# Performance work log

Hardware: AMD Instinct MI355X
Metric: run time of the kernel (lower is better)

The kernel has to match this reference:

```python
import jax, jax.numpy as jnp
import numpy as np
from jax import lax

B, H, V, L = 128, 256, 130, 100  # batch, hidden_size, vocab per stream, decode length


def _gru(x, h, wih, whh, bih, bhh):
    # torch.nn.GRUCell math
    gi = x @ wih.T + bih
    gh = h @ whh.T + bhh
    ir, iz, inn = jnp.split(gi, 3, axis=-1)
    hr, hz, hn = jnp.split(gh, 3, axis=-1)
    r = jax.nn.sigmoid(ir + hr)
    u = jax.nn.sigmoid(iz + hz)
    n = jnp.tanh(inn + r * hn)
    return (1.0 - u) * n + u * h


def _forward(z, gru1_wih, gru1_whh, gru1_bih, gru1_bhh,
             gru2_wih, gru2_whh, gru2_bih, gru2_bhh,
             ctx_wih, ctx_whh, ctx_bih, ctx_bhh,
             out_w, out_b, hid_w, hid_b, emb, length):
    b = z.shape[0]
    hidden = jnp.tanh(z @ hid_w.T + hid_b)                      # [B,H]
    h3 = jnp.broadcast_to(hidden[None], (3, b, hidden.shape[-1]))
    note0 = jnp.broadcast_to(emb[:, 0][:, None, :], (3, b, emb.shape[-1]))  # embed index 0
    vgru = jax.vmap(_gru)  # over the 3 parallel streams

    def step(carry, _):
        g1h, g2h, context, note = carry
        zb = jnp.broadcast_to(z[None], note.shape)
        g1h = vgru(jnp.concatenate([note, zb], -1), g1h,
                   gru1_wih, gru1_whh, gru1_bih, gru1_bhh)       # [3,B,H]
        unroll = g1h
        logits = []
        for i in range(3):  # fixed structural unroll (3 streams)
            ctx_in = jnp.concatenate([unroll[0], unroll[1], unroll[2]], -1)  # [B,3H]
            context = _gru(ctx_in, context, ctx_wih, ctx_whh, ctx_bih, ctx_bhh)
            h2 = _gru(jnp.concatenate([context, z], -1), g2h[i],
                      gru2_wih[i], gru2_whh[i], gru2_bih[i], gru2_bhh[i])
            g2h = g2h.at[i].set(h2)
            lg = (unroll[i] + h2) @ out_w[i].T + out_b[i]        # [B,V]
            logits.append(lg)
            ni = emb[i][jnp.argmax(lg, axis=-1)]                 # greedy sample -> embed
            note = note.at[i].set(ni)
            # NOTE: original code uses self.gru1[1] here (fixed index 1) -- kept faithful
            unroll = unroll.at[i].set(_gru(jnp.concatenate([ni, z], -1), unroll[i],
                                           gru1_wih[1], gru1_whh[1], gru1_bih[1], gru1_bhh[1]))
        return (g1h, g2h, context, note), jnp.stack(logits)     # [3,B,V]

    _, ys = lax.scan(step, (h3, h3, hidden, note0), None, length=length)
    return jnp.transpose(ys, (1, 2, 0, 3))                      # [3,B,L,V]


def setup_inputs() -> dict:
    key = jax.random.key(0)
    ks = jax.random.split(key, 18)
    s = 0.05
    n = lambda k, shp: jax.random.normal(k, shp, jnp.float32) * s
    return {
        "z": jax.random.normal(ks[0], (B, H), jnp.float32),
        "gru1_wih": n(ks[1], (3, 3 * H, 2 * H)),
        "gru1_whh": n(ks[2], (3, 3 * H, H)),
        "gru1_bih": n(ks[3], (3, 3 * H)),
        "gru1_bhh": n(ks[4], (3, 3 * H)),
        "gru2_wih": n(ks[5], (3, 3 * H, 2 * H)),
        "gru2_whh": n(ks[6], (3, 3 * H, H)),
        "gru2_bih": n(ks[7], (3, 3 * H)),
        "gru2_bhh": n(ks[8], (3, 3 * H)),
        "ctx_wih": n(ks[9], (3 * H, 3 * H)),
        "ctx_whh": n(ks[10], (3 * H, H)),
        "ctx_bih": n(ks[11], (3 * H,)),
        "ctx_bhh": n(ks[12], (3 * H,)),
        "out_w": n(ks[13], (3, V, H)),
        "out_b": n(ks[14], (3, V)),
        "hid_w": n(ks[15], (H, H)),
        "hid_b": n(ks[16], (H,)),
        "emb": n(ks[17], (3, V, H)),
        "length": L,
    }


def reference(z, gru1_wih, gru1_whh, gru1_bih, gru1_bhh,
              gru2_wih, gru2_whh, gru2_bih, gru2_bhh,
              ctx_wih, ctx_whh, ctx_bih, ctx_bhh,
              out_w, out_b, hid_w, hid_b, emb, length):
    return _forward(z, gru1_wih, gru1_whh, gru1_bih, gru1_bhh,
                    gru2_wih, gru2_whh, gru2_bih, gru2_bhh,
                    ctx_wih, ctx_whh, ctx_bih, ctx_bhh,
                    out_w, out_b, hid_w, hid_b, emb, length)
```

## Files before the change

### kernel.cpp

```cpp
#include <hip/hip_runtime.h>
#include <math.h>

#define B 128
#define H 256
#define V 130
#define L 100
#define G3 768
#define BH (B*H)
#define NWG 256
#define NT 512

#define OFF_FLAGS 0
#define OFF_XRANK 512
#define OFF_CLAIM 640
#define OFF_HID   1024
#define OFF_Z1    (OFF_HID + BH)
#define OFF_Z2    (OFF_Z1 + 3*B*G3)
#define OFF_G1HA  (OFF_Z2 + 3*B*G3)
#define OFF_G1HB  (OFF_G1HA + 3*BH)
#define OFF_H2A   (OFF_G1HB + 3*BH)
#define OFF_H2B   (OFF_H2A + 3*BH)
#define OFF_CTXA  (OFF_H2B + 3*BH)
#define OFF_CTXB  (OFF_CTXA + BH)
#define OFF_U0    (OFF_CTXB + BH)
#define OFF_U1    (OFF_U0 + 3*BH)
#define OFF_NOTE  (OFF_U1 + 3*BH)

typedef float v4f __attribute__((ext_vector_type(4)));

__device__ __forceinline__ float sigmoidf_(float x) { return 1.0f / (1.0f + expf(-x)); }

__device__ __forceinline__ v4f load_coh4(const float* p) {
  v4f v;
  asm volatile("global_load_dwordx4 %0, %1, off sc0 sc1" : "=v"(v) : "v"(p) : "memory");
  return v;
}
__device__ __forceinline__ void store_coh(float* p, float v) {
  asm volatile("global_store_dword %0, %1, off sc0 sc1" :: "v"(p), "v"(v) : "memory");
}
__device__ __forceinline__ void store_coh4(float* p, v4f v) {
  asm volatile("global_store_dwordx4 %0, %1, off sc0 sc1" :: "v"(p), "v"(v) : "memory");
}
__device__ __forceinline__ void waitvm0() {
  asm volatile("s_waitcnt vmcnt(0)" ::: "memory");
}

__device__ __forceinline__ void grid_barrier(int* cnt, int epoch) {
  waitvm0();
  __syncthreads();
  if (threadIdx.x == 0)
    __hip_atomic_fetch_add(cnt + (blockIdx.x & 31) * 16, 1,
                           __ATOMIC_RELAXED, __HIP_MEMORY_SCOPE_AGENT);
  if (threadIdx.x < 64) {
    const int lane = threadIdx.x;
    const int target = epoch * NWG;
    for (;;) {
      int c = 0;
      if (lane < 32)
        c = __hip_atomic_load(cnt + lane * 16, __ATOMIC_RELAXED, __HIP_MEMORY_SCOPE_AGENT);
      c += __shfl_xor(c, 1);
      c += __shfl_xor(c, 2);
      c += __shfl_xor(c, 4);
      c += __shfl_xor(c, 8);
      c += __shfl_xor(c, 16);
      if (__shfl(c, 0) >= target) break;
      __builtin_amdgcn_s_sleep(2);
    }
  }
  __syncthreads();
}

template <int NCHUNK>
__device__ void gru_phase(
    const float* __restrict__ xc0, const float* __restrict__ xc1,
    const float* __restrict__ xc2, const float* __restrict__ xc3,
    const float* __restrict__ wih, int wih_stride,
    const float* __restrict__ whh,
    const float* __restrict__ zadd,
    const float* __restrict__ bih,
    const float* __restrict__ bhh,
    float* __restrict__ out0, float* __restrict__ out1,
    float* smem, int row0, int col0, int tid)
{
  const float* xc[4] = {xc0, xc1, xc2, xc3};
  v4f stg[2 * NCHUNK];
#pragma unroll
  for (int c = 0; c < NCHUNK; ++c) {
#pragma unroll
    for (int q = 0; q < 2; ++q) {
      const int idx = q * NT + tid;
      const int rr = idx >> 6;
      const int k4 = (idx & 63) << 2;
      stg[c * 2 + q] = load_coh4(xc[c] + (size_t)(row0 + rr) * H + k4);
    }
  }
  __syncthreads();
  waitvm0();
#pragma unroll
  for (int c = 0; c < NCHUNK; ++c) {
#pragma unroll
    for (int q = 0; q < 2; ++q) {
      const int idx = q * NT + tid;
      const int rr = idx >> 6;
      const int k4 = (idx & 63) << 2;
      *reinterpret_cast<v4f*>(smem + c * 4160 + rr * 260 + k4) = stg[c * 2 + q];
    }
  }
  __syncthreads();

  const int kq = tid & 3;
  const int row_l = (tid >> 2) & 15;
  const int col_l = tid >> 6;
  const int col = col0 + col_l;

  const int kstart = kq * (NCHUNK * 64);
  const int c = kstart >> 8;
  const int koff = kstart & 255;
  const bool is_ih = (c < NCHUNK - 1);

  const float* wb;
  int wstr;
  if (is_ih) { wstr = wih_stride; wb = wih + (size_t)col * wstr + (c * 256 + koff); }
  else       { wstr = 256;        wb = whh + (size_t)col * 256 + koff; }
  const float* wR = wb;
  const float* wZ = wb + (size_t)256 * wstr;
  const float* wN = wb + (size_t)512 * wstr;
  const float* xr = smem + c * 4160 + row_l * 260 + koff;

  float aR = 0.f, aZ = 0.f, aN = 0.f;
  const int klen = NCHUNK * 64;
#pragma unroll 8
  for (int k = 0; k < klen; k += 4) {
    float4 xv = *reinterpret_cast<const float4*>(xr + k);
    float4 vR = *reinterpret_cast<const float4*>(wR + k);
    float4 vZ = *reinterpret_cast<const float4*>(wZ + k);
    float4 vN = *reinterpret_cast<const float4*>(wN + k);
    aR += xv.x * vR.x; aR += xv.y * vR.y; aR += xv.z * vR.z; aR += xv.w * vR.w;
    aZ += xv.x * vZ.x; aZ += xv.y * vZ.y; aZ += xv.z * vZ.z; aZ += xv.w * vZ.w;
    aN += xv.x * vN.x; aN += xv.y * vN.y; aN += xv.z * vN.z; aN += xv.w * vN.w;
  }
  float aNi = is_ih ? aN : 0.f;
  float aNh = is_ih ? 0.f : aN;
#pragma unroll
  for (int m = 1; m <= 2; m <<= 1) {
    aR  += __shfl_xor(aR, m);
    aZ  += __shfl_xor(aZ, m);
    aNi += __shfl_xor(aNi, m);
    aNh += __shfl_xor(aNh, m);
  }
  if (kq == 0) {
    float bR, bZ, bN;
    if (zadd) {
      const float* zp = zadd + (size_t)(row0 + row_l) * G3;
      bR = zp[col]; bZ = zp[256 + col]; bN = zp[512 + col];
    } else {
      bR = bih[col]; bZ = bih[256 + col]; bN = bih[512 + col];
    }
    const float hR = bhh[col], hZ = bhh[256 + col], hN = bhh[512 + col];
    const float hold = smem[(NCHUNK - 1) * 4160 + row_l * 260 + col];
    const float rg = sigmoidf_(aR + bR + hR);
    const float ug = sigmoidf_(aZ + bZ + hZ);
    const float ng = tanhf(aNi + bN + rg * (aNh + hN));
    const float hnew = (1.f - ug) * ng + ug * hold;
    const size_t o = (size_t)(row0 + row_l) * H + col;
    store_coh(out0 + o, hnew);
    if (out1) store_coh(out1 + o, hnew);
  }
}

__device__ void out_phase(
    const float* __restrict__ u0i, const float* __restrict__ h2i,
    const float* __restrict__ ow, const float* __restrict__ ob,
    const float* __restrict__ embi,
    float* __restrict__ note_i, float* __restrict__ outp,
    float* smem, int* sidx, int w, int tid)
{
  if (w >= B) return;
  const int row = w;
  v4f a4, b4;
  if (tid < 64) {
    a4 = load_coh4(u0i + (size_t)row * H + tid * 4);
    b4 = load_coh4(h2i + (size_t)row * H + tid * 4);
  }
  __syncthreads();
  if (tid < 64) {
    waitvm0();
    v4f s4 = a4 + b4;
    *reinterpret_cast<v4f*>(smem + tid * 4) = s4;
  }
  __syncthreads();

  const int v = tid >> 2, kq = tid & 3;
#pragma unroll
  for (int p = 0; p < 2; ++p) {
    const int vv = v + p * 128;
    if (vv < V) {
      const float* wrow = ow + (size_t)vv * H + kq * 64;
      const float* xr = smem + kq * 64;
      float acc = 0.f;
#pragma unroll 4
      for (int k = 0; k < 64; k += 4) {
        float4 xv = *reinterpret_cast<const float4*>(xr + k);
        float4 wv = *reinterpret_cast<const float4*>(wrow + k);
        acc += xv.x * wv.x; acc += xv.y * wv.y; acc += xv.z * wv.z; acc += xv.w * wv.w;
      }
      acc += __shfl_xor(acc, 1);
      acc += __shfl_xor(acc, 2);
      if (kq == 0) {
        acc += ob[vv];
        outp[vv] = acc;
        smem[260 * 4 + vv] = acc;
      }
    }
  }
  __syncthreads();
  if (tid < 64) {
    float* vals = smem + 260 * 4;
    float bv = vals[tid]; int bi = tid;
    float c1 = vals[64 + tid];
    if (c1 > bv) { bv = c1; bi = 64 + tid; }
    if (tid < 2) { float c2 = vals[128 + tid]; if (c2 > bv) { bv = c2; bi = 128 + tid; } }
#pragma unroll
    for (int off = 32; off; off >>= 1) {
      float ov = __shfl_down(bv, off);
      int oi = __shfl_down(bi, off);
      if (ov > bv || (ov == bv && oi < bi)) { bv = ov; bi = oi; }
    }
    if (tid == 0) *sidx = bi;
  }
  __syncthreads();
  const int idx = *sidx;
  if (tid < 64) {
    const float* erow = embi + (size_t)idx * H + tid * 4;
    v4f e = *reinterpret_cast<const v4f*>(erow);
    store_coh4(note_i + (size_t)row * H + tid * 4, e);
  }
}

__global__ __launch_bounds__(NT) void decoder_persistent(
    const float* __restrict__ g1wih, const float* __restrict__ g1whh,
    const float* __restrict__ g1bhh,
    const float* __restrict__ g2wih, const float* __restrict__ g2whh,
    const float* __restrict__ g2bhh,
    const float* __restrict__ cwih, const float* __restrict__ cwhh,
    const float* __restrict__ cbih, const float* __restrict__ cbhh,
    const float* __restrict__ outw, const float* __restrict__ outb,
    const float* __restrict__ emb,
    float* __restrict__ out, float* __restrict__ wsf)
{
  __shared__ float smem[20608];
  __shared__ int sidx;
  __shared__ int s_tile;
  int* cnt   = reinterpret_cast<int*>(wsf) + OFF_FLAGS;
  int* xrank = reinterpret_cast<int*>(wsf) + OFF_XRANK;
  int* claim = reinterpret_cast<int*>(wsf) + OFF_CLAIM;
  float* Z1   = wsf + OFF_Z1;
  float* Z2   = wsf + OFF_Z2;
  float* g1h[2] = {wsf + OFF_G1HA, wsf + OFF_G1HB};
  float* h2b[2] = {wsf + OFF_H2A,  wsf + OFF_H2B};
  float* ctx[2] = {wsf + OFF_CTXA, wsf + OFF_CTXB};
  float* U0   = wsf + OFF_U0;
  float* U1   = wsf + OFF_U1;
  float* note = wsf + OFF_NOTE;

  const int w = blockIdx.x, tid = threadIdx.x;

  if (tid == 0) {
    int xcc;
    asm("s_getreg_b32 %0, hwreg(20, 0, 32)" : "=s"(xcc));
    xcc &= 7;
    int rk = __hip_atomic_fetch_add(xrank + xcc * 16, 1,
                                    __ATOMIC_RELAXED, __HIP_MEMORY_SCOPE_AGENT);
    int tile = (rk < 32) ? (xcc * 32 + rk) : (w & 255);
    for (;;) {
      if (atomicCAS(claim + tile, 0, 1) == 0) break;
      tile = (tile + 1) & 255;
    }
    s_tile = tile;
  }
  __syncthreads();
  const int tile = s_tile;
  const int col0 = (tile >> 5) * 32 + (tile & 3) * 8;
  const int row0 = ((tile >> 2) & 7) * 16;
  int ep = 0;

  for (int t = 0; t < L; ++t) {
    const int rbk = t & 1, wbk = (t + 1) & 1;
    for (int s = 0; s < 3; ++s) {
      gru_phase<2>(note + (size_t)s * BH, g1h[rbk] + (size_t)s * BH, nullptr, nullptr,
                   g1wih + (size_t)s * G3 * 512, 512, g1whh + (size_t)s * G3 * H,
                   Z1 + (size_t)s * B * G3, nullptr, g1bhh + (size_t)s * G3,
                   g1h[wbk] + (size_t)s * BH, U0 + (size_t)s * BH,
                   smem, row0, col0, tid);
    }
    grid_barrier(cnt, ++ep);
    for (int i = 0; i < 3; ++i) {
      const int j = 3 * t + i;
      const float* us0 = (0 < i ? U1 : U0) + 0 * BH;
      const float* us1 = (1 < i ? U1 : U0) + 1 * BH;
      const float* us2 = (2 < i ? U1 : U0) + 2 * BH;
      gru_phase<4>(us0, us1, us2, ctx[j & 1],
                   cwih, G3, cwhh,
                   nullptr, cbih, cbhh,
                   ctx[(j + 1) & 1], nullptr,
                   smem, row0, col0, tid);
      grid_barrier(cnt, ++ep);
      gru_phase<2>(ctx[(j + 1) & 1], h2b[rbk] + (size_t)i * BH, nullptr, nullptr,
                   g2wih + (size_t)i * G3 * 512, 512, g2whh + (size_t)i * G3 * H,
                   Z2 + (size_t)i * B * G3, nullptr, g2bhh + (size_t)i * G3,
                   h2b[wbk] + (size_t)i * BH, nullptr,
                   smem, row0, col0, tid);
      grid_barrier(cnt, ++ep);
      out_phase(U0 + (size_t)i * BH, h2b[wbk] + (size_t)i * BH,
                outw + (size_t)i * V * H, outb + (size_t)i * V, emb + (size_t)i * V * H,
                note + (size_t)i * BH,
                out + (size_t)i * B * L * V + (size_t)w * L * V + (size_t)t * V,
                smem, &sidx, w, tid);
      grid_barrier(cnt, ++ep);
      gru_phase<2>(note + (size_t)i * BH, U0 + (size_t)i * BH, nullptr, nullptr,
                   g1wih + (size_t)1 * G3 * 512, 512, g1whh + (size_t)1 * G3 * H,
                   Z1 + (size_t)1 * B * G3, nullptr, g1bhh + (size_t)1 * G3,
                   U1 + (size_t)i * BH, nullptr,
                   smem, row0, col0, tid);
      grid_barrier(cnt, ++ep);
    }
  }
}

__global__ __launch_bounds__(256) void hid_kernel(
    const float* __restrict__ z, const float* __restrict__ hw,
    const float* __restrict__ hb, float* __restrict__ hidden)
{
  __shared__ float xs[32][260];
  const int tid = threadIdx.x;
  const int r = tid & 31, hc = tid >> 5;
  const int row0 = blockIdx.y * 32;
  const int col = blockIdx.x * 8 + hc;
  for (int jj = tid; jj < 32 * 64; jj += 256) {
    const int rr = jj >> 6, k4 = (jj & 63) << 2;
    *reinterpret_cast<float4*>(&xs[rr][k4]) =
        *reinterpret_cast<const float4*>(z + (size_t)(row0 + rr) * H + k4);
  }
  __syncthreads();
  float acc = 0.f;
  const float* wrow = hw + (size_t)col * H;
#pragma unroll 8
  for (int k = 0; k < 256; k += 4) {
    const float4 xv = *reinterpret_cast<const float4*>(&xs[r][k]);
    const float4 wv = *reinterpret_cast<const float4*>(wrow + k);
    acc += xv.x * wv.x; acc += xv.y * wv.y; acc += xv.z * wv.z; acc += xv.w * wv.w;
  }
  hidden[(size_t)(row0 + r) * H + col] = tanhf(acc + hb[col]);
}

__global__ __launch_bounds__(256) void zpre_kernel(
    const float* __restrict__ z, const float* __restrict__ wih,
    const float* __restrict__ bih, float* __restrict__ zout)
{
  __shared__ float xs[32][260];
  const int tid = threadIdx.x;
  const int r = tid & 31, hc = tid >> 5;
  const int row0 = blockIdx.y * 32;
  const int gr = blockIdx.x * 8 + hc;
  const int s = gr / G3;
  const int g = gr - s * G3;
  for (int jj = tid; jj < 32 * 64; jj += 256) {
    const int rr = jj >> 6, k4 = (jj & 63) << 2;
    *reinterpret_cast<float4*>(&xs[rr][k4]) =
        *reinterpret_cast<const float4*>(z + (size_t)(row0 + rr) * H + k4);
  }
  __syncthreads();
  float acc = 0.f;
  const float* wrow = wih + (size_t)gr * 512 + 256;
#pragma unroll 8
  for (int k = 0; k < 256; k += 4) {
    const float4 xv = *reinterpret_cast<const float4*>(&xs[r][k]);
    const float4 wv = *reinterpret_cast<const float4*>(wrow + k);
    acc += xv.x * wv.x; acc += xv.y * wv.y; acc += xv.z * wv.z; acc += xv.w * wv.w;
  }
  zout[((size_t)(s * B + row0 + r)) * G3 + g] = acc + bih[gr];
}

__global__ __launch_bounds__(256) void init_copy(
    const float* __restrict__ hidden, float* __restrict__ g1h0,
    float* __restrict__ h20, float* __restrict__ ctx0)
{
  const int e = blockIdx.x * 256 + threadIdx.x;
  const float v = hidden[e];
  ctx0[e] = v;
  for (int s = 0; s < 3; ++s) {
    g1h0[(size_t)s * BH + e] = v;
    h20[(size_t)s * BH + e] = v;
  }
}

__global__ __launch_bounds__(256) void init_note(
    const float* __restrict__ emb, float* __restrict__ note)
{
  const int e = blockIdx.x * 256 + threadIdx.x;
  const int s = e / BH;
  const int c = e & (H - 1);
  note[e] = emb[(size_t)s * V * H + c];
}

__global__ void zero_flags(int* flags) { flags[threadIdx.x] = 0; }

extern "C" void kernel_launch(void* const* d_in, const int* in_sizes, int n_in,
                              void* d_out, int out_size, void* d_ws, size_t ws_size,
                              hipStream_t stream) {
  const float* z     = (const float*)d_in[0];
  const float* g1wih = (const float*)d_in[1];
  const float* g1whh = (const float*)d_in[2];
  const float* g1bih = (const float*)d_in[3];
  const float* g1bhh = (const float*)d_in[4];
  const float* g2wih = (const float*)d_in[5];
  const float* g2whh = (const float*)d_in[6];
  const float* g2bih = (const float*)d_in[7];
  const float* g2bhh = (const float*)d_in[8];
  const float* cwih  = (const float*)d_in[9];
  const float* cwhh  = (const float*)d_in[10];
  const float* cbih  = (const float*)d_in[11];
  const float* cbhh  = (const float*)d_in[12];
  const float* outw  = (const float*)d_in[13];
  const float* outb  = (const float*)d_in[14];
  const float* hidw  = (const float*)d_in[15];
  const float* hidb  = (const float*)d_in[16];
  const float* emb   = (const float*)d_in[17];
  float* out = (float*)d_out;
  float* wsf = (float*)d_ws;
  int* flags = (int*)d_ws;

  const dim3 blk(256);
  hid_kernel<<<dim3(32, 4), blk, 0, stream>>>(z, hidw, hidb, wsf + OFF_HID);
  zpre_kernel<<<dim3(288, 4), blk, 0, stream>>>(z, g1wih, g1bih, wsf + OFF_Z1);
  zpre_kernel<<<dim3(288, 4), blk, 0, stream>>>(z, g2wih, g2bih, wsf + OFF_Z2);
  init_copy<<<128, blk, 0, stream>>>(wsf + OFF_HID, wsf + OFF_G1HA,
                                     wsf + OFF_H2A, wsf + OFF_CTXA);
  init_note<<<384, blk, 0, stream>>>(emb, wsf + OFF_NOTE);
  zero_flags<<<1, 1024, 0, stream>>>(flags);

  decoder_persistent<<<NWG, NT, 0, stream>>>(
      g1wih, g1whh, g1bhh, g2wih, g2whh, g2bhh,
      cwih, cwhh, cbih, cbhh, outw, outb, emb, out, wsf);
}
```

Baseline: 39.43 ms.

## Replace grid-wide barrier with per-row-group barriers and retile for 1024 threads

Each workgroup now owns 4 batch rows across 32 columns, and workgroups tile the batch into 32 independent row groups. Because the recurrence is row-independent, a grid-wide barrier is replaced by a barrier among just the 8 workgroups that share the same rows, which is meant to cut sync latency. Threads per block double to 1024, the K-split widens to 8 lanes, and shared memory gets a padded layout to avoid bank conflicts. The output phase is spread so that 4 of the 8 workgroups in each group handle one row each. The risk is lower per-block occupancy and more shuffle reduction steps.

Result: faster. 37.78 ms (-4.2%).

```diff
diff --git a/kernel.cpp b/kernel.cpp
--- a/kernel.cpp
+++ b/kernel.cpp
@@ -8,7 +8,7 @@
 #define G3 768
 #define BH (B*H)
 #define NWG 256
-#define NT 512
+#define NT 1024
 
 #define OFF_FLAGS 0
 #define OFF_XRANK 512
@@ -45,27 +45,14 @@
   asm volatile("s_waitcnt vmcnt(0)" ::: "memory");
 }
 
-__device__ __forceinline__ void grid_barrier(int* cnt, int epoch) {
+__device__ __forceinline__ void group_barrier(int* cnt, int grp, int target, int tid) {
   waitvm0();
   __syncthreads();
-  if (threadIdx.x == 0)
-    __hip_atomic_fetch_add(cnt + (blockIdx.x & 31) * 16, 1,
-                           __ATOMIC_RELAXED, __HIP_MEMORY_SCOPE_AGENT);
-  if (threadIdx.x < 64) {
-    const int lane = threadIdx.x;
-    const int target = epoch * NWG;
-    for (;;) {
-      int c = 0;
-      if (lane < 32)
-        c = __hip_atomic_load(cnt + lane * 16, __ATOMIC_RELAXED, __HIP_MEMORY_SCOPE_AGENT);
-      c += __shfl_xor(c, 1);
-      c += __shfl_xor(c, 2);
-      c += __shfl_xor(c, 4);
-      c += __shfl_xor(c, 8);
-      c += __shfl_xor(c, 16);
-      if (__shfl(c, 0) >= target) break;
-      __builtin_amdgcn_s_sleep(2);
-    }
+  if (tid == 0) {
+    int* c = cnt + grp * 16;
+    __hip_atomic_fetch_add(c, 1, __ATOMIC_RELAXED, __HIP_MEMORY_SCOPE_AGENT);
+    while (__hip_atomic_load(c, __ATOMIC_RELAXED, __HIP_MEMORY_SCOPE_AGENT) < target)
+      __builtin_amdgcn_s_sleep(1);
   }
   __syncthreads();
 }
@@ -83,39 +70,33 @@
     float* smem, int row0, int col0, int tid)
 {
   const float* xc[4] = {xc0, xc1, xc2, xc3};
-  v4f stg[2 * NCHUNK];
-#pragma unroll
-  for (int c = 0; c < NCHUNK; ++c) {
-#pragma unroll
-    for (int q = 0; q < 2; ++q) {
-      const int idx = q * NT + tid;
-      const int rr = idx >> 6;
-      const int k4 = (idx & 63) << 2;
-      stg[c * 2 + q] = load_coh4(xc[c] + (size_t)(row0 + rr) * H + k4);
-    }
+  v4f stg;
+  int sc = 0, srr = 0, sk4 = 0;
+  const int nldv = NCHUNK * 256;
+  if (tid < nldv) {
+    sc  = tid >> 8;
+    const int r = tid & 255;
+    srr = r >> 6;
+    sk4 = (r & 63) << 2;
+    stg = load_coh4(xc[sc] + (size_t)(row0 + srr) * H + sk4);
   }
   __syncthreads();
   waitvm0();
-#pragma unroll
-  for (int c = 0; c < NCHUNK; ++c) {
-#pragma unroll
-    for (int q = 0; q < 2; ++q) {
-      const int idx = q * NT + tid;
-      const int rr = idx >> 6;
-      const int k4 = (idx & 63) << 2;
-      *reinterpret_cast<v4f*>(smem + c * 4160 + rr * 260 + k4) = stg[c * 2 + q];
-    }
-  }
-  __syncthreads();
-
-  const int kq = tid & 3;
-  const int row_l = (tid >> 2) & 15;
-  const int col_l = tid >> 6;
-  const int col = col0 + col_l;
-
-  const int kstart = kq * (NCHUNK * 64);
-  const int c = kstart >> 8;
-  const int koff = kstart & 255;
+  if (tid < nldv) {
+    const int sw = (sk4 >> 6) * 65 + (sk4 & 63);
+    *reinterpret_cast<v4f*>(smem + sc * 1040 + srr * 260 + sw) = stg;
+  }
+  __syncthreads();
+
+  const int kq    = tid & 7;
+  const int row_l = (tid >> 3) & 3;
+  const int col_l = tid >> 5;
+  const int col   = col0 + col_l;
+
+  const int klen   = NCHUNK * 32;
+  const int kstart = kq * klen;
+  const int c      = kstart >> 8;
+  const int koff   = kstart & 255;
   const bool is_ih = (c < NCHUNK - 1);
 
   const float* wb;
@@ -125,24 +106,33 @@
   const float* wR = wb;
   const float* wZ = wb + (size_t)256 * wstr;
   const float* wN = wb + (size_t)512 * wstr;
-  const float* xr = smem + c * 4160 + row_l * 260 + koff;
+  const float* xrow = smem + c * 1040 + row_l * 260;
 
   float aR = 0.f, aZ = 0.f, aN = 0.f;
-  const int klen = NCHUNK * 64;
+  const int nkb = klen >> 6;
+#pragma unroll
+  for (int kb = 0; kb < (klen == 64 ? 1 : 2); ++kb) {
+    const int kof2 = koff + kb * 64;
+    const float* xb = xrow + (kof2 >> 6) * 65;
+    const float* wRb = wR + kb * 64;
+    const float* wZb = wZ + kb * 64;
+    const float* wNb = wN + kb * 64;
 #pragma unroll 8
-  for (int k = 0; k < klen; k += 4) {
-    float4 xv = *reinterpret_cast<const float4*>(xr + k);
-    float4 vR = *reinterpret_cast<const float4*>(wR + k);
-    float4 vZ = *reinterpret_cast<const float4*>(wZ + k);
-    float4 vN = *reinterpret_cast<const float4*>(wN + k);
-    aR += xv.x * vR.x; aR += xv.y * vR.y; aR += xv.z * vR.z; aR += xv.w * vR.w;
-    aZ += xv.x * vZ.x; aZ += xv.y * vZ.y; aZ += xv.z * vZ.z; aZ += xv.w * vZ.w;
-    aN += xv.x * vN.x; aN += xv.y * vN.y; aN += xv.z * vN.z; aN += xv.w * vN.w;
-  }
+    for (int k = 0; k < 64; k += 4) {
+      v4f xv = *reinterpret_cast<const v4f*>(xb + k);
+      v4f vR = *reinterpret_cast<const v4f*>(wRb + k);
+      v4f vZ = *reinterpret_cast<const v4f*>(wZb + k);
+      v4f vN = *reinterpret_cast<const v4f*>(wNb + k);
+      aR += xv.x * vR.x; aR += xv.y * vR.y; aR += xv.z * vR.z; aR += xv.w * vR.w;
+      aZ += xv.x * vZ.x; aZ += xv.y * vZ.y; aZ += xv.z * vZ.z; aZ += xv.w * vZ.w;
+      aN += xv.x * vN.x; aN += xv.y * vN.y; aN += xv.z * vN.z; aN += xv.w * vN.w;
+    }
+  }
+  (void)nkb;
   float aNi = is_ih ? aN : 0.f;
   float aNh = is_ih ? 0.f : aN;
 #pragma unroll
-  for (int m = 1; m <= 2; m <<= 1) {
+  for (int m = 1; m <= 4; m <<= 1) {
     aR  += __shfl_xor(aR, m);
     aZ  += __shfl_xor(aZ, m);
     aNi += __shfl_xor(aNi, m);
@@ -157,7 +147,7 @@
       bR = bih[col]; bZ = bih[256 + col]; bN = bih[512 + col];
     }
     const float hR = bhh[col], hZ = bhh[256 + col], hN = bhh[512 + col];
-    const float hold = smem[(NCHUNK - 1) * 4160 + row_l * 260 + col];
+    const float hold = smem[(NCHUNK - 1) * 1040 + row_l * 260 + (col >> 6) * 65 + (col & 63)];
     const float rg = sigmoidf_(aR + bR + hR);
     const float ug = sigmoidf_(aZ + bZ + hZ);
     const float ng = tanhf(aNi + bN + rg * (aNh + hN));
@@ -173,10 +163,9 @@
     const float* __restrict__ ow, const float* __restrict__ ob,
     const float* __restrict__ embi,
     float* __restrict__ note_i, float* __restrict__ outp,
-    float* smem, int* sidx, int w, int tid)
-{
-  if (w >= B) return;
-  const int row = w;
+    float* smem, int* sidx, int row, bool active, int tid)
+{
+  if (!active) return;
   v4f a4, b4;
   if (tid < 64) {
     a4 = load_coh4(u0i + (size_t)row * H + tid * 4);
@@ -185,37 +174,32 @@
   __syncthreads();
   if (tid < 64) {
     waitvm0();
-    v4f s4 = a4 + b4;
-    *reinterpret_cast<v4f*>(smem + tid * 4) = s4;
+    *reinterpret_cast<v4f*>(smem + tid * 4) = a4 + b4;
   }
   __syncthreads();
 
   const int v = tid >> 2, kq = tid & 3;
-#pragma unroll
-  for (int p = 0; p < 2; ++p) {
-    const int vv = v + p * 128;
-    if (vv < V) {
-      const float* wrow = ow + (size_t)vv * H + kq * 64;
-      const float* xr = smem + kq * 64;
-      float acc = 0.f;
-#pragma unroll 4
-      for (int k = 0; k < 64; k += 4) {
-        float4 xv = *reinterpret_cast<const float4*>(xr + k);
-        float4 wv = *reinterpret_cast<const float4*>(wrow + k);
-        acc += xv.x * wv.x; acc += xv.y * wv.y; acc += xv.z * wv.z; acc += xv.w * wv.w;
-      }
-      acc += __shfl_xor(acc, 1);
-      acc += __shfl_xor(acc, 2);
-      if (kq == 0) {
-        acc += ob[vv];
-        outp[vv] = acc;
-        smem[260 * 4 + vv] = acc;
-      }
+  if (v < V) {
+    const float* wrow = ow + (size_t)v * H + kq * 64;
+    const float* xr = smem + kq * 64;
+    float acc = 0.f;
+#pragma unroll 8
+    for (int k = 0; k < 64; k += 4) {
+      v4f xv = *reinterpret_cast<const v4f*>(xr + k);
+      v4f wv = *reinterpret_cast<const v4f*>(wrow + k);
+      acc += xv.x * wv.x; acc += xv.y * wv.y; acc += xv.z * wv.z; acc += xv.w * wv.w;
+    }
+    acc += __shfl_xor(acc, 1);
+    acc += __shfl_xor(acc, 2);
+    if (kq == 0) {
+      acc += ob[v];
+      outp[v] = acc;
+      smem[256 + v] = acc;
     }
   }
   __syncthreads();
   if (tid < 64) {
-    float* vals = smem + 260 * 4;
+    float* vals = smem + 256;
     float bv = vals[tid]; int bi = tid;
     float c1 = vals[64 + tid];
     if (c1 > bv) { bv = c1; bi = 64 + tid; }
@@ -231,8 +215,7 @@
   __syncthreads();
   const int idx = *sidx;
   if (tid < 64) {
-    const float* erow = embi + (size_t)idx * H + tid * 4;
-    v4f e = *reinterpret_cast<const v4f*>(erow);
+    v4f e = *reinterpret_cast<const v4f*>(embi + (size_t)idx * H + tid * 4);
     store_coh4(note_i + (size_t)row * H + tid * 4, e);
   }
 }
@@ -263,7 +246,7 @@
   float* U1   = wsf + OFF_U1;
   float* note = wsf + OFF_NOTE;
 
-  const int w = blockIdx.x, tid = threadIdx.x;
+  const int tid = threadIdx.x;
 
   if (tid == 0) {
     int xcc;
@@ -271,7 +254,7 @@
     xcc &= 7;
     int rk = __hip_atomic_fetch_add(xrank + xcc * 16, 1,
                                     __ATOMIC_RELAXED, __HIP_MEMORY_SCOPE_AGENT);
-    int tile = (rk < 32) ? (xcc * 32 + rk) : (w & 255);
+    int tile = (rk < 32) ? (xcc * 32 + rk) : ((int)blockIdx.x & 255);
     for (;;) {
       if (atomicCAS(claim + tile, 0, 1) == 0) break;
       tile = (tile + 1) & 255;
@@ -280,8 +263,12 @@
   }
   __syncthreads();
   const int tile = s_tile;
-  const int col0 = (tile >> 5) * 32 + (tile & 3) * 8;
-  const int row0 = ((tile >> 2) & 7) * 16;
+  const int xs = tile >> 5;
+  const int g  = tile & 31;
+  const int col0 = xs * 32;
+  const int row0 = g * 4;
+  const bool oact = (xs < 4);
+  const int orow = row0 + xs;
   int ep = 0;
 
   for (int t = 0; t < L; ++t) {
@@ -293,7 +280,7 @@
                    g1h[wbk] + (size_t)s * BH, U0 + (size_t)s * BH,
                    smem, row0, col0, tid);
     }
-    grid_barrier(cnt, ++ep);
+    group_barrier(cnt, g, (++ep) * 8, tid);
     for (int i = 0; i < 3; ++i) {
       const int j = 3 * t + i;
       const float* us0 = (0 < i ? U1 : U0) + 0 * BH;
@@ -304,25 +291,25 @@
                    nullptr, cbih, cbhh,
                    ctx[(j + 1) & 1], nullptr,
                    smem, row0, col0, tid);
-      grid_barrier(cnt, ++ep);
+      group_barrier(cnt, g, (++ep) * 8, tid);
       gru_phase<2>(ctx[(j + 1) & 1], h2b[rbk] + (size_t)i * BH, nullptr, nullptr,
                    g2wih + (size_t)i * G3 * 512, 512, g2whh + (size_t)i * G3 * H,
                    Z2 + (size_t)i * B * G3, nullptr, g2bhh + (size_t)i * G3,
                    h2b[wbk] + (size_t)i * BH, nullptr,
                    smem, row0, col0, tid);
-      grid_barrier(cnt, ++ep);
+      group_barrier(cnt, g, (++ep) * 8, tid);
       out_phase(U0 + (size_t)i * BH, h2b[wbk] + (size_t)i * BH,
                 outw + (size_t)i * V * H, outb + (size_t)i * V, emb + (size_t)i * V * H,
                 note + (size_t)i * BH,
-                out + (size_t)i * B * L * V + (size_t)w * L * V + (size_t)t * V,
-                smem, &sidx, w, tid);
-      grid_barrier(cnt, ++ep);
+                out + (size_t)i * B * L * V + (size_t)orow * L * V + (size_t)t * V,
+                smem, &sidx, orow, oact, tid);
+      group_barrier(cnt, g, (++ep) * 8, tid);
       gru_phase<2>(note + (size_t)i * BH, U0 + (size_t)i * BH, nullptr, nullptr,
                    g1wih + (size_t)1 * G3 * 512, 512, g1whh + (size_t)1 * G3 * H,
                    Z1 + (size_t)1 * B * G3, nullptr, g1bhh + (size_t)1 * G3,
                    U1 + (size_t)i * BH, nullptr,
                    smem, row0, col0, tid);
-      grid_barrier(cnt, ++ep);
+      group_barrier(cnt, g, (++ep) * 8, tid);
     }
   }
 }
@@ -363,7 +350,7 @@
   const int row0 = blockIdx.y * 32;
   const int gr = blockIdx.x * 8 + hc;
   const int s = gr / G3;
-  const int g = gr - s * G3;
+  const int gg = gr - s * G3;
   for (int jj = tid; jj < 32 * 64; jj += 256) {
     const int rr = jj >> 6, k4 = (jj & 63) << 2;
     *reinterpret_cast<float4*>(&xs[rr][k4]) =
@@ -378,7 +365,7 @@
     const float4 wv = *reinterpret_cast<const float4*>(wrow + k);
     acc += xv.x * wv.x; acc += xv.y * wv.y; acc += xv.z * wv.z; acc += xv.w * wv.w;
   }
-  zout[((size_t)(s * B + row0 + r)) * G3 + g] = acc + bih[gr];
+  zout[((size_t)(s * B + row0 + r)) * G3 + gg] = acc + bih[gr];
 }
 
 __global__ __launch_bounds__(256) void init_copy(
```
